# Kernel tuning notes

Measured on AMD Instinct MI355X. Metric: run time of the kernel, lower is better.

## Reference

```python
import jax, jax.numpy as jnp
import numpy as np

M, D1, D2, E = 8, 32, 32, 256      # batch, board dims, embedding_dim
K = 2                               # selection_size
L = 16384                           # number of selection moves
NSPECIAL, SIDX, NPLAYERS, H = 32, 8, 4, 256


def setup_inputs() -> dict:
    key = jax.random.key(0)
    ks = jax.random.split(key, 14)
    din = E * (1 + K)
    inp = {
        "embedding": jax.random.normal(ks[0], (M, D1, D2, E), jnp.float32),
        "cls_embedding": jax.random.normal(ks[1], (M, E), jnp.float32),
        "selection_moves": jax.random.randint(ks[2], (L, K, 2), 0, D1, dtype=jnp.int32),
        "special_move_idxs": jax.random.randint(ks[3], (SIDX,), 0, NSPECIAL, dtype=jnp.int32),
        # policy head: single Linear(din, 1) (hidden_layers=None)
        "Wp": jax.random.normal(ks[4], (din, 1), jnp.float32) / np.sqrt(din).astype(np.float32),
        "bp": jnp.zeros((1,), jnp.float32),
        # value head: Linear(E,H) -> ReLU -> Linear(H, num_players)
        "Wv1": jax.random.normal(ks[5], (E, H), jnp.float32) / np.sqrt(E).astype(np.float32),
        "bv1": jnp.zeros((H,), jnp.float32),
        "Wv2": jax.random.normal(ks[6], (H, NPLAYERS), jnp.float32) / np.sqrt(H).astype(np.float32),
        "bv2": jnp.zeros((NPLAYERS,), jnp.float32),
        # special head: Linear(E,H) -> ReLU -> Linear(H, num_special_moves)
        "Ws1": jax.random.normal(ks[7], (E, H), jnp.float32) / np.sqrt(E).astype(np.float32),
        "bs1": jnp.zeros((H,), jnp.float32),
        "Ws2": jax.random.normal(ks[8], (H, NSPECIAL), jnp.float32) / np.sqrt(H).astype(np.float32),
        "bs2": jnp.zeros((NSPECIAL,), jnp.float32),
    }
    return inp


def reference(embedding, cls_embedding, selection_moves, special_move_idxs,
              Wp, bp, Wv1, bv1, Wv2, bv2, Ws1, bs1, Ws2, bs2):
    Mb, Ed = cls_embedding.shape
    # irregular gather: (M, L, K, E) from (M, D1, D2, E) via 2-D move indices
    gath = embedding[:, selection_moves[..., 0], selection_moves[..., 1], :]
    Lm = gath.shape[1]
    # concat the K selected embeddings then the cls embedding -> (M, L, (K+1)*E)
    sel = jnp.concatenate(
        [gath.reshape(Mb, Lm, -1),
         jnp.broadcast_to(cls_embedding[:, None, :], (Mb, Lm, Ed))], axis=-1)
    policy = (sel @ Wp + bp).reshape(Mb, -1)                       # (M, L)
    special_all = jax.nn.relu(cls_embedding @ Ws1 + bs1) @ Ws2 + bs2
    special = special_all[:, special_move_idxs]                    # (M, S)
    policy = jnp.concatenate([policy, special], axis=1)            # (M, L+S)
    value = jax.nn.relu(cls_embedding @ Wv1 + bv1) @ Wv2 + bv2     # (M, num_players)
    return policy, value
```

## Files before the change

kernel.cpp:

```cpp
#include <hip/hip_runtime.h>

#define M_ 8
#define D1_ 32
#define D2_ 32
#define E_ 256
#define K_ 2
#define L_ 16384
#define NSPECIAL_ 32
#define SIDX_ 8
#define NPLAYERS_ 4
#define H_ 256
#define P_ (D1_ * D2_)
#define POL_COLS (L_ + SIDX_)

#define NCHUNK 16
#define CHUNK_E (E_ / NCHUNK)

#define WS_A 0
#define WS_B (M_ * P_)
#define WS_BASE (2 * M_ * P_)
#define WS_PART (2 * M_ * P_ + 256)
#define WS_NEED_BYTES ((WS_PART + 2 * M_ * NCHUNK * H_) * 4)

__global__ __launch_bounds__(256) void k_fused1(
    const float* __restrict__ emb, const float* __restrict__ cls,
    const float* __restrict__ Wp, const float* __restrict__ bp,
    const float* __restrict__ Ws1, const float* __restrict__ Wv1,
    float* __restrict__ ws)
{
    const int blk = blockIdx.x;
    const int tid = threadIdx.x;

    if (blk < 2048) {
        const int wave = tid >> 6, lane = tid & 63;
        const int b = blk * 4 + wave;
        const float4 v  = ((const float4*)(emb + (size_t)b * E_))[lane];
        const float4 w0 = ((const float4*)(Wp))[lane];
        const float4 w1 = ((const float4*)(Wp + E_))[lane];
        float a  = v.x * w0.x + v.y * w0.y + v.z * w0.z + v.w * w0.w;
        float bb = v.x * w1.x + v.y * w1.y + v.z * w1.z + v.w * w1.w;
        #pragma unroll
        for (int off = 32; off > 0; off >>= 1) {
            a  += __shfl_down(a,  off, 64);
            bb += __shfl_down(bb, off, 64);
        }
        if (lane == 0) { ws[WS_A + b] = a; ws[WS_B + b] = bb; }
    } else if (blk < 2050) {
        const int wave = tid >> 6, lane = tid & 63;
        const int m = (blk - 2048) * 4 + wave;
        const float4 v = ((const float4*)(cls + (size_t)m * E_))[lane];
        const float4 w = ((const float4*)(Wp + 2 * E_))[lane];
        float a = v.x * w.x + v.y * w.y + v.z * w.z + v.w * w.w;
        #pragma unroll
        for (int off = 32; off > 0; off >>= 1) a += __shfl_down(a, off, 64);
        if (lane == 0) ws[WS_BASE + m] = a + bp[0];
    } else {
        const int idx  = blk - 2050;
        const int head = idx >> 7;
        const int rem  = idx & 127;
        const int m    = rem >> 4;
        const int c    = rem & 15;
        const float* __restrict__ W1 = head ? Wv1 : Ws1;
        const int e0 = c * CHUNK_E;
        const float* __restrict__ cm = cls + (size_t)m * E_ + e0;
        float acc = 0.f;
        #pragma unroll
        for (int i = 0; i < CHUNK_E; ++i)
            acc = fmaf(cm[i], W1[(size_t)(e0 + i) * H_ + tid], acc);
        ws[WS_PART + (size_t)((head * M_ + m) * NCHUNK + c) * H_ + tid] = acc;
    }
}

__global__ __launch_bounds__(256) void k_fused2(
    const int* __restrict__ sm, const float* __restrict__ ws,
    const int* __restrict__ sidx,
    const float* __restrict__ bs1, const float* __restrict__ bv1,
    const float* __restrict__ Ws2, const float* __restrict__ bs2,
    const float* __restrict__ Wv2, const float* __restrict__ bv2,
    float* __restrict__ out)
{
    __shared__ float sh[2 * P_ + 64];
    const int blk = blockIdx.x;
    const int t = threadIdx.x;

    if (blk < 512) {
        float* As = sh;
        float* Bs = sh + P_;
        const int m = blk >> 6;
        ((float4*)As)[t] = ((const float4*)(ws + WS_A + (size_t)m * P_))[t];
        ((float4*)Bs)[t] = ((const float4*)(ws + WS_B + (size_t)m * P_))[t];
        const float bm = ws[WS_BASE + m];
        __syncthreads();
        const int l = ((blk & 63) << 8) + t;
        const int4 s = ((const int4*)sm)[l];
        out[(size_t)m * POL_COLS + l] = As[s.x * D2_ + s.y] + Bs[s.z * D2_ + s.w] + bm;
    } else {
        float* hid = sh;
        float* red = sh + H_;
        float* sp  = sh + 2 * H_;
        const int idx  = blk - 512;
        const int head = idx >> 3;
        const int m    = idx & 7;

        float acc = head ? bv1[t] : bs1[t];
        const float* __restrict__ pb =
            ws + WS_PART + (size_t)((head * M_ + m) * NCHUNK) * H_ + t;
        #pragma unroll
        for (int c = 0; c < NCHUNK; ++c) acc += pb[c * H_];
        hid[t] = fmaxf(acc, 0.f);
        __syncthreads();

        if (head == 0) {
            const int ns = t & 31, c = t >> 5;
            float p = 0.f;
            #pragma unroll
            for (int i = 0; i < 32; ++i) {
                const int h = c * 32 + i;
                p = fmaf(hid[h], Ws2[(size_t)h * NSPECIAL_ + ns], p);
            }
            red[t] = p;
            __syncthreads();
            if (t < NSPECIAL_) {
                float s = bs2[t];
                #pragma unroll
                for (int c2 = 0; c2 < 8; ++c2) s += red[c2 * 32 + t];
                sp[t] = s;
            }
            __syncthreads();
            if (t < SIDX_)
                out[(size_t)m * POL_COLS + L_ + t] = sp[sidx[t]];
        } else {
            if (t < 128) {
                const int np = t & 3, c = t >> 2;
                float p = 0.f;
                #pragma unroll
                for (int i = 0; i < 8; ++i) {
                    const int h = c * 8 + i;
                    p = fmaf(hid[h], Wv2[(size_t)h * NPLAYERS_ + np], p);
                }
                red[t] = p;
            }
            __syncthreads();
            if (t < NPLAYERS_) {
                float s = bv2[t];
                #pragma unroll
                for (int c2 = 0; c2 < 32; ++c2) s += red[c2 * 4 + t];
                out[(size_t)M_ * POL_COLS + (size_t)m * NPLAYERS_ + t] = s;
            }
        }
    }
}

__global__ __launch_bounds__(256) void k_heads_fallback(
    const float* __restrict__ cls, const int* __restrict__ sidx,
    const float* __restrict__ Wv1, const float* __restrict__ bv1,
    const float* __restrict__ Wv2, const float* __restrict__ bv2,
    const float* __restrict__ Ws1, const float* __restrict__ bs1,
    const float* __restrict__ Ws2, const float* __restrict__ bs2,
    float* __restrict__ out)
{
    __shared__ float cl[E_];
    __shared__ float hs[H_];
    __shared__ float hv[H_];
    __shared__ float sp[NSPECIAL_];
    const int m = blockIdx.x;
    const int t = threadIdx.x;
    cl[t] = cls[(size_t)m * E_ + t];
    __syncthreads();
    float as = bs1[t], av = bv1[t];
    #pragma unroll 4
    for (int e = 0; e < E_; ++e) {
        const float c = cl[e];
        as = fmaf(c, Ws1[(size_t)e * H_ + t], as);
        av = fmaf(c, Wv1[(size_t)e * H_ + t], av);
    }
    hs[t] = fmaxf(as, 0.f);
    hv[t] = fmaxf(av, 0.f);
    __syncthreads();
    if (t < NSPECIAL_) {
        float acc = bs2[t];
        for (int h = 0; h < H_; ++h) acc = fmaf(hs[h], Ws2[(size_t)h * NSPECIAL_ + t], acc);
        sp[t] = acc;
    } else if (t >= 64 && t < 64 + NPLAYERS_) {
        const int n = t - 64;
        float acc = bv2[n];
        for (int h = 0; h < H_; ++h) acc = fmaf(hv[h], Wv2[(size_t)h * NPLAYERS_ + n], acc);
        out[(size_t)M_ * POL_COLS + (size_t)m * NPLAYERS_ + n] = acc;
    }
    __syncthreads();
    if (t < SIDX_) out[(size_t)m * POL_COLS + L_ + t] = sp[sidx[t]];
}

__global__ __launch_bounds__(64) void k_tables_fallback(
    const float* __restrict__ emb, const float* __restrict__ cls,
    const float* __restrict__ Wp, const float* __restrict__ bp,
    float* __restrict__ ws)
{
    const int b = blockIdx.x;
    const int lane = threadIdx.x;
    if (b < M_ * P_) {
        const float4 v  = ((const float4*)(emb + (size_t)b * E_))[lane];
        const float4 w0 = ((const float4*)(Wp))[lane];
        const float4 w1 = ((const float4*)(Wp + E_))[lane];
        float a  = v.x * w0.x + v.y * w0.y + v.z * w0.z + v.w * w0.w;
        float bb = v.x * w1.x + v.y * w1.y + v.z * w1.z + v.w * w1.w;
        #pragma unroll
        for (int off = 32; off > 0; off >>= 1) {
            a  += __shfl_down(a,  off, 64);
            bb += __shfl_down(bb, off, 64);
        }
        if (lane == 0) { ws[WS_A + b] = a; ws[WS_B + b] = bb; }
    } else {
        const int m = b - M_ * P_;
        const float4 v = ((const float4*)(cls + (size_t)m * E_))[lane];
        const float4 w = ((const float4*)(Wp + 2 * E_))[lane];
        float a = v.x * w.x + v.y * w.y + v.z * w.z + v.w * w.w;
        #pragma unroll
        for (int off = 32; off > 0; off >>= 1) a += __shfl_down(a, off, 64);
        if (lane == 0) ws[WS_BASE + m] = a + bp[0];
    }
}

__global__ __launch_bounds__(256) void k_policy_fallback(
    const int* __restrict__ sm, const float* __restrict__ ws,
    float* __restrict__ out)
{
    __shared__ float As[P_], Bs[P_];
    const int b = blockIdx.x;
    const int m = b >> 6;
    ((float4*)As)[threadIdx.x] = ((const float4*)(ws + WS_A + (size_t)m * P_))[threadIdx.x];
    ((float4*)Bs)[threadIdx.x] = ((const float4*)(ws + WS_B + (size_t)m * P_))[threadIdx.x];
    const float bm = ws[WS_BASE + m];
    __syncthreads();
    const int l = ((b & 63) << 8) + threadIdx.x;
    const int4 s = ((const int4*)sm)[l];
    out[(size_t)m * POL_COLS + l] = As[s.x * D2_ + s.y] + Bs[s.z * D2_ + s.w] + bm;
}

extern "C" void kernel_launch(void* const* d_in, const int* in_sizes, int n_in,
                              void* d_out, int out_size, void* d_ws, size_t ws_size,
                              hipStream_t stream) {
    const float* emb  = (const float*)d_in[0];
    const float* cls  = (const float*)d_in[1];
    const int*   sm   = (const int*)d_in[2];
    const int*   sidx = (const int*)d_in[3];
    const float* Wp   = (const float*)d_in[4];
    const float* bp   = (const float*)d_in[5];
    const float* Wv1  = (const float*)d_in[6];
    const float* bv1  = (const float*)d_in[7];
    const float* Wv2  = (const float*)d_in[8];
    const float* bv2  = (const float*)d_in[9];
    const float* Ws1  = (const float*)d_in[10];
    const float* bs1  = (const float*)d_in[11];
    const float* Ws2  = (const float*)d_in[12];
    const float* bs2  = (const float*)d_in[13];
    float* out = (float*)d_out;
    float* ws  = (float*)d_ws;

    if (ws_size >= (size_t)WS_NEED_BYTES) {
        k_fused1<<<2050 + 2 * M_ * NCHUNK, 256, 0, stream>>>(
            emb, cls, Wp, bp, Ws1, Wv1, ws);
        k_fused2<<<512 + 16, 256, 0, stream>>>(
            sm, ws, sidx, bs1, bv1, Ws2, bs2, Wv2, bv2, out);
    } else {
        k_tables_fallback<<<M_ * P_ + M_, 64, 0, stream>>>(emb, cls, Wp, bp, ws);
        k_heads_fallback<<<M_, 256, 0, stream>>>(cls, sidx, Wv1, bv1, Wv2, bv2,
                                                 Ws1, bs1, Ws2, bs2, out);
        k_policy_fallback<<<M_ * (L_ / 256), 256, 0, stream>>>(sm, ws, out);
    }
}
```

Before: 85.89 us.

## Merge two-kernel pipeline into one cooperative kernel with grid sync

Replaces the two back-to-back launches (table/partial-head kernel, then gather/head kernel) with a single cooperative kernel of 528 blocks. Phase one runs as a grid-stride job loop in which each wave handles four embedding rows using 16-lane sub-groups. A grid-wide sync then separates it from the original gather and head-finishing phase. This aims to remove one kernel launch and the gap between kernels, at the cost of a grid barrier and fewer blocks for phase one. The small-workspace fallback path is removed, and the two-kernel path is kept only for when the cooperative launch fails.

```diff
diff --git a/kernel.cpp b/kernel.cpp
--- a/kernel.cpp
+++ b/kernel.cpp
@@ -1,4 +1,6 @@
 #include <hip/hip_runtime.h>
+#include <hip/hip_cooperative_groups.h>
+namespace cg = cooperative_groups;
 
 #define M_ 8
 #define D1_ 32
@@ -22,67 +24,80 @@
 #define WS_PART (2 * M_ * P_ + 256)
 #define WS_NEED_BYTES ((WS_PART + 2 * M_ * NCHUNK * H_) * 4)
 
-__global__ __launch_bounds__(256) void k_fused1(
+#define GRID_ 528
+#define NJOB_AB 512
+#define JOB_BASE 512
+#define NJOBA 769
+
+__global__ __launch_bounds__(256) void k_pv_coop(
     const float* __restrict__ emb, const float* __restrict__ cls,
+    const int* __restrict__ sm, const int* __restrict__ sidx,
     const float* __restrict__ Wp, const float* __restrict__ bp,
     const float* __restrict__ Ws1, const float* __restrict__ Wv1,
-    float* __restrict__ ws)
-{
-    const int blk = blockIdx.x;
-    const int tid = threadIdx.x;
-
-    if (blk < 2048) {
-        const int wave = tid >> 6, lane = tid & 63;
-        const int b = blk * 4 + wave;
-        const float4 v  = ((const float4*)(emb + (size_t)b * E_))[lane];
-        const float4 w0 = ((const float4*)(Wp))[lane];
-        const float4 w1 = ((const float4*)(Wp + E_))[lane];
-        float a  = v.x * w0.x + v.y * w0.y + v.z * w0.z + v.w * w0.w;
-        float bb = v.x * w1.x + v.y * w1.y + v.z * w1.z + v.w * w1.w;
-        #pragma unroll
-        for (int off = 32; off > 0; off >>= 1) {
-            a  += __shfl_down(a,  off, 64);
-            bb += __shfl_down(bb, off, 64);
-        }
-        if (lane == 0) { ws[WS_A + b] = a; ws[WS_B + b] = bb; }
-    } else if (blk < 2050) {
-        const int wave = tid >> 6, lane = tid & 63;
-        const int m = (blk - 2048) * 4 + wave;
-        const float4 v = ((const float4*)(cls + (size_t)m * E_))[lane];
-        const float4 w = ((const float4*)(Wp + 2 * E_))[lane];
-        float a = v.x * w.x + v.y * w.y + v.z * w.z + v.w * w.w;
-        #pragma unroll
-        for (int off = 32; off > 0; off >>= 1) a += __shfl_down(a, off, 64);
-        if (lane == 0) ws[WS_BASE + m] = a + bp[0];
-    } else {
-        const int idx  = blk - 2050;
-        const int head = idx >> 7;
-        const int rem  = idx & 127;
-        const int m    = rem >> 4;
-        const int c    = rem & 15;
-        const float* __restrict__ W1 = head ? Wv1 : Ws1;
-        const int e0 = c * CHUNK_E;
-        const float* __restrict__ cm = cls + (size_t)m * E_ + e0;
-        float acc = 0.f;
-        #pragma unroll
-        for (int i = 0; i < CHUNK_E; ++i)
-            acc = fmaf(cm[i], W1[(size_t)(e0 + i) * H_ + tid], acc);
-        ws[WS_PART + (size_t)((head * M_ + m) * NCHUNK + c) * H_ + tid] = acc;
-    }
-}
-
-__global__ __launch_bounds__(256) void k_fused2(
-    const int* __restrict__ sm, const float* __restrict__ ws,
-    const int* __restrict__ sidx,
     const float* __restrict__ bs1, const float* __restrict__ bv1,
     const float* __restrict__ Ws2, const float* __restrict__ bs2,
     const float* __restrict__ Wv2, const float* __restrict__ bv2,
-    float* __restrict__ out)
+    float* __restrict__ ws, float* __restrict__ out)
 {
     __shared__ float sh[2 * P_ + 64];
+    const int t = threadIdx.x;
+    const int wave = t >> 6, lane = t & 63;
+    const int sub = lane >> 4, li = lane & 15;
+
+    for (int job = blockIdx.x; job < NJOBA; job += GRID_) {
+        if (job < NJOB_AB) {
+            const int row = job * 16 + wave * 4 + sub;
+            const float* __restrict__ rp = emb + (size_t)row * E_;
+            float a = 0.f, b = 0.f;
+            #pragma unroll
+            for (int it = 0; it < 4; ++it) {
+                const float4 v  = ((const float4*)rp)[li + 16 * it];
+                const float4 w0 = ((const float4*)Wp)[li + 16 * it];
+                const float4 w1 = ((const float4*)(Wp + E_))[li + 16 * it];
+                a += v.x * w0.x + v.y * w0.y + v.z * w0.z + v.w * w0.w;
+                b += v.x * w1.x + v.y * w1.y + v.z * w1.z + v.w * w1.w;
+            }
+            #pragma unroll
+            for (int off = 8; off > 0; off >>= 1) {
+                a += __shfl_down(a, off, 16);
+                b += __shfl_down(b, off, 16);
+            }
+            if (li == 0) { ws[WS_A + row] = a; ws[WS_B + row] = b; }
+        } else if (job == JOB_BASE) {
+            if (wave < 2) {
+                const int m = wave * 4 + sub;
+                const float* __restrict__ rp = cls + (size_t)m * E_;
+                float a = 0.f;
+                #pragma unroll
+                for (int it = 0; it < 4; ++it) {
+                    const float4 v = ((const float4*)rp)[li + 16 * it];
+                    const float4 w = ((const float4*)(Wp + 2 * E_))[li + 16 * it];
+                    a += v.x * w.x + v.y * w.y + v.z * w.z + v.w * w.w;
+                }
+                #pragma unroll
+                for (int off = 8; off > 0; off >>= 1) a += __shfl_down(a, off, 16);
+                if (li == 0) ws[WS_BASE + m] = a + bp[0];
+            }
+        } else {
+            const int idx  = job - JOB_BASE - 1;
+            const int head = idx >> 7;
+            const int rem  = idx & 127;
+            const int m    = rem >> 4;
+            const int c    = rem & 15;
+            const float* __restrict__ W1 = head ? Wv1 : Ws1;
+            const int e0 = c * CHUNK_E;
+            const float* __restrict__ cm = cls + (size_t)m * E_ + e0;
+            float acc = 0.f;
+            #pragma unroll
+            for (int i = 0; i < CHUNK_E; ++i)
+                acc = fmaf(cm[i], W1[(size_t)(e0 + i) * H_ + t], acc);
+            ws[WS_PART + (size_t)((head * M_ + m) * NCHUNK + c) * H_ + t] = acc;
+        }
+    }
+
+    cg::this_grid().sync();
+
     const int blk = blockIdx.x;
-    const int t = threadIdx.x;
-
     if (blk < 512) {
         float* As = sh;
         float* Bs = sh + P_;
@@ -151,54 +166,18 @@
     }
 }
 
-__global__ __launch_bounds__(256) void k_heads_fallback(
-    const float* __restrict__ cls, const int* __restrict__ sidx,
-    const float* __restrict__ Wv1, const float* __restrict__ bv1,
-    const float* __restrict__ Wv2, const float* __restrict__ bv2,
-    const float* __restrict__ Ws1, const float* __restrict__ bs1,
-    const float* __restrict__ Ws2, const float* __restrict__ bs2,
-    float* __restrict__ out)
-{
-    __shared__ float cl[E_];
-    __shared__ float hs[H_];
-    __shared__ float hv[H_];
-    __shared__ float sp[NSPECIAL_];
-    const int m = blockIdx.x;
-    const int t = threadIdx.x;
-    cl[t] = cls[(size_t)m * E_ + t];
-    __syncthreads();
-    float as = bs1[t], av = bv1[t];
-    #pragma unroll 4
-    for (int e = 0; e < E_; ++e) {
-        const float c = cl[e];
-        as = fmaf(c, Ws1[(size_t)e * H_ + t], as);
-        av = fmaf(c, Wv1[(size_t)e * H_ + t], av);
-    }
-    hs[t] = fmaxf(as, 0.f);
-    hv[t] = fmaxf(av, 0.f);
-    __syncthreads();
-    if (t < NSPECIAL_) {
-        float acc = bs2[t];
-        for (int h = 0; h < H_; ++h) acc = fmaf(hs[h], Ws2[(size_t)h * NSPECIAL_ + t], acc);
-        sp[t] = acc;
-    } else if (t >= 64 && t < 64 + NPLAYERS_) {
-        const int n = t - 64;
-        float acc = bv2[n];
-        for (int h = 0; h < H_; ++h) acc = fmaf(hv[h], Wv2[(size_t)h * NPLAYERS_ + n], acc);
-        out[(size_t)M_ * POL_COLS + (size_t)m * NPLAYERS_ + n] = acc;
-    }
-    __syncthreads();
-    if (t < SIDX_) out[(size_t)m * POL_COLS + L_ + t] = sp[sidx[t]];
-}
-
-__global__ __launch_bounds__(64) void k_tables_fallback(
+__global__ __launch_bounds__(256) void k_fused1(
     const float* __restrict__ emb, const float* __restrict__ cls,
     const float* __restrict__ Wp, const float* __restrict__ bp,
+    const float* __restrict__ Ws1, const float* __restrict__ Wv1,
     float* __restrict__ ws)
 {
-    const int b = blockIdx.x;
-    const int lane = threadIdx.x;
-    if (b < M_ * P_) {
+    const int blk = blockIdx.x;
+    const int tid = threadIdx.x;
+
+    if (blk < 2048) {
+        const int wave = tid >> 6, lane = tid & 63;
+        const int b = blk * 4 + wave;
         const float4 v  = ((const float4*)(emb + (size_t)b * E_))[lane];
         const float4 w0 = ((const float4*)(Wp))[lane];
         const float4 w1 = ((const float4*)(Wp + E_))[lane];
@@ -210,31 +189,110 @@
             bb += __shfl_down(bb, off, 64);
         }
         if (lane == 0) { ws[WS_A + b] = a; ws[WS_B + b] = bb; }
-    } else {
-        const int m = b - M_ * P_;
+    } else if (blk < 2050) {
+        const int wave = tid >> 6, lane = tid & 63;
+        const int m = (blk - 2048) * 4 + wave;
         const float4 v = ((const float4*)(cls + (size_t)m * E_))[lane];
         const float4 w = ((const float4*)(Wp + 2 * E_))[lane];
         float a = v.x * w.x + v.y * w.y + v.z * w.z + v.w * w.w;
         #pragma unroll
         for (int off = 32; off > 0; off >>= 1) a += __shfl_down(a, off, 64);
         if (lane == 0) ws[WS_BASE + m] = a + bp[0];
+    } else {
+        const int idx  = blk - 2050;
+        const int head = idx >> 7;
+        const int rem  = idx & 127;
+        const int m    = rem >> 4;
+        const int c    = rem & 15;
+        const float* __restrict__ W1 = head ? Wv1 : Ws1;
+        const int e0 = c * CHUNK_E;
+        const float* __restrict__ cm = cls + (size_t)m * E_ + e0;
+        float acc = 0.f;
+        #pragma unroll
+        for (int i = 0; i < CHUNK_E; ++i)
+            acc = fmaf(cm[i], W1[(size_t)(e0 + i) * H_ + tid], acc);
+        ws[WS_PART + (size_t)((head * M_ + m) * NCHUNK + c) * H_ + tid] = acc;
     }
 }
 
-__global__ __launch_bounds__(256) void k_policy_fallback(
+__global__ __launch_bounds__(256) void k_fused2(
     const int* __restrict__ sm, const float* __restrict__ ws,
+    const int* __restrict__ sidx,
+    const float* __restrict__ bs1, const float* __restrict__ bv1,
+    const float* __restrict__ Ws2, const float* __restrict__ bs2,
+    const float* __restrict__ Wv2, const float* __restrict__ bv2,
     float* __restrict__ out)
 {
-    __shared__ float As[P_], Bs[P_];
-    const int b = blockIdx.x;
-    const int m = b >> 6;
-    ((float4*)As)[threadIdx.x] = ((const float4*)(ws + WS_A + (size_t)m * P_))[threadIdx.x];
-    ((float4*)Bs)[threadIdx.x] = ((const float4*)(ws + WS_B + (size_t)m * P_))[threadIdx.x];
-    const float bm = ws[WS_BASE + m];
-    __syncthreads();
-    const int l = ((b & 63) << 8) + threadIdx.x;
-    const int4 s = ((const int4*)sm)[l];
-    out[(size_t)m * POL_COLS + l] = As[s.x * D2_ + s.y] + Bs[s.z * D2_ + s.w] + bm;
+    __shared__ float sh[2 * P_ + 64];
+    const int blk = blockIdx.x;
+    const int t = threadIdx.x;
+
+    if (blk < 512) {
+        float* As = sh;
+        float* Bs = sh + P_;
+        const int m = blk >> 6;
+        ((float4*)As)[t] = ((const float4*)(ws + WS_A + (size_t)m * P_))[t];
+        ((float4*)Bs)[t] = ((const float4*)(ws + WS_B + (size_t)m * P_))[t];
+        const float bm = ws[WS_BASE + m];
+        __syncthreads();
+        const int l = ((blk & 63) << 8) + t;
+        const int4 s = ((const int4*)sm)[l];
+        out[(size_t)m * POL_COLS + l] = As[s.x * D2_ + s.y] + Bs[s.z * D2_ + s.w] + bm;
+    } else {
+        float* hid = sh;
+        float* red = sh + H_;
+        float* sp  = sh + 2 * H_;
+        const int idx  = blk - 512;
+        const int head = idx >> 3;
+        const int m    = idx & 7;
+
+        float acc = head ? bv1[t] : bs1[t];
+        const float* __restrict__ pb =
+            ws + WS_PART + (size_t)((head * M_ + m) * NCHUNK) * H_ + t;
+        #pragma unroll
+        for (int c = 0; c < NCHUNK; ++c) acc += pb[c * H_];
+        hid[t] = fmaxf(acc, 0.f);
+        __syncthreads();
+
+        if (head == 0) {
+            const int ns = t & 31, c = t >> 5;
+            float p = 0.f;
+            #pragma unroll
+            for (int i = 0; i < 32; ++i) {
+                const int h = c * 32 + i;
+                p = fmaf(hid[h], Ws2[(size_t)h * NSPECIAL_ + ns], p);
+            }
+            red[t] = p;
+            __syncthreads();
+            if (t < NSPECIAL_) {
+                float s = bs2[t];
+                #pragma unroll
+                for (int c2 = 0; c2 < 8; ++c2) s += red[c2 * 32 + t];
+                sp[t] = s;
+            }
+            __syncthreads();
+            if (t < SIDX_)
+                out[(size_t)m * POL_COLS + L_ + t] = sp[sidx[t]];
+        } else {
+            if (t < 128) {
+                const int np = t & 3, c = t >> 2;
+                float p = 0.f;
+                #pragma unroll
+                for (int i = 0; i < 8; ++i) {
+                    const int h = c * 8 + i;
+                    p = fmaf(hid[h], Wv2[(size_t)h * NPLAYERS_ + np], p);
+                }
+                red[t] = p;
+            }
+            __syncthreads();
+            if (t < NPLAYERS_) {
+                float s = bv2[t];
+                #pragma unroll
+                for (int c2 = 0; c2 < 32; ++c2) s += red[c2 * 4 + t];
+                out[(size_t)M_ * POL_COLS + (size_t)m * NPLAYERS_ + t] = s;
+            }
+        }
+    }
 }
 
 extern "C" void kernel_launch(void* const* d_in, const int* in_sizes, int n_in,
@@ -257,15 +315,21 @@
     float* out = (float*)d_out;
     float* ws  = (float*)d_ws;
 
+    hipError_t err = hipErrorUnknown;
     if (ws_size >= (size_t)WS_NEED_BYTES) {
+        void* args[] = {
+            (void*)&emb, (void*)&cls, (void*)&sm, (void*)&sidx,
+            (void*)&Wp,  (void*)&bp,  (void*)&Ws1, (void*)&Wv1,
+            (void*)&bs1, (void*)&bv1, (void*)&Ws2, (void*)&bs2,
+            (void*)&Wv2, (void*)&bv2, (void*)&ws,  (void*)&out };
+        err = hipLaunchCooperativeKernel((const void*)k_pv_coop,
+                                         dim3(GRID_), dim3(256),
+                                         args, 0, stream);
+    }
+    if (err != hipSuccess && ws_size >= (size_t)WS_NEED_BYTES) {
         k_fused1<<<2050 + 2 * M_ * NCHUNK, 256, 0, stream>>>(
             emb, cls, Wp, bp, Ws1, Wv1, ws);
         k_fused2<<<512 + 16, 256, 0, stream>>>(
             sm, ws, sidx, bs1, bv1, Ws2, bs2, Wv2, bv2, out);
-    } else {
-        k_tables_fallback<<<M_ * P_ + M_, 64, 0, stream>>>(emb, cls, Wp, bp, ws);
-        k_heads_fallback<<<M_, 256, 0, stream>>>(cls, sidx, Wv1, bv1, Wv2, bv2,
-                                                 Ws1, bs1, Ws2, bs2, out);
-        k_policy_fallback<<<M_ * (L_ / 256), 256, 0, stream>>>(sm, ws, out);
     }
 }
```

Result: slower. 151.7 us (+76.6%).
